# Optimization experiments

Hardware: AMD Instinct MI355X
Metric: run time of the kernel (lower is better)

The kernel has to match this reference:

```python
import jax, jax.numpy as jnp
import numpy as np

M, N, DIM, B = 64, 64, 512, 4096
SIGMA = max(M, N) / 2.0  # default sigma in BaseSOM.__init__


def setup_inputs() -> dict:
    key = jax.random.key(0)
    k1, k2 = jax.random.split(key)
    batch = jax.random.normal(k1, (B, DIM), dtype=jnp.float32)
    weights = jax.random.uniform(k2, (M * N, DIM), dtype=jnp.float32)
    # grid locations [(i, j) for i in range(M) for j in range(N)]
    ii, jj = jnp.meshgrid(jnp.arange(M), jnp.arange(N), indexing="ij")
    locations = jnp.stack([ii.reshape(-1), jj.reshape(-1)], axis=1).astype(jnp.int64)
    return {
        "batch": batch,
        "weights": weights,
        "locations": locations,
        "decay_rate": 1000,
        "it": 100,
    }


def reference(batch, weights, locations, decay_rate, it):
    # Squared Euclidean distances (argmin is identical to argmin of cdist p=2).
    x2 = jnp.sum(batch * batch, axis=1, keepdims=True)          # [B, 1]
    w2 = jnp.sum(weights * weights, axis=1)[None, :]            # [1, MN]
    d2 = x2 - 2.0 * (batch @ weights.T) + w2                    # [B, MN]
    bmu_indices = jnp.argmin(d2, axis=1)                        # [B]
    bmu_loc = locations[bmu_indices]                            # [B, 2]
    lr = jnp.exp(-jnp.float32(it) / jnp.float32(decay_rate))
    sigma_op = jnp.float32(SIGMA) * lr
    # [B, MN, 2] grid offsets -> squared grid distance [B, MN]
    diff = locations[None, :, :].astype(jnp.float32) - bmu_loc[:, None, :].astype(jnp.float32)
    dist_sq = jnp.sum(diff * diff, axis=2)
    return jnp.exp(-dist_sq / (sigma_op * sigma_op))
```

## Files before the change

### kernel.cpp

```cpp
#include <hip/hip_runtime.h>
#include <cfloat>

#define DIMK 512
#define MN   4096
#define BATCH 4096
#define BK 32
#define NGRP 1024

typedef _Float16 half8_t __attribute__((ext_vector_type(8)));
typedef _Float16 half4_t __attribute__((ext_vector_type(4)));
typedef float f32x4 __attribute__((ext_vector_type(4)));

#define GLD16(gp, lp) __builtin_amdgcn_global_load_lds( \
    (const __attribute__((address_space(1))) void*)(gp), \
    (__attribute__((address_space(3))) void*)(lp), 16, 0, 0)

__global__ __launch_bounds__(256) void convert_kernel(
        const float* __restrict__ X, const float* __restrict__ W,
        _Float16* __restrict__ Xh, _Float16* __restrict__ Wh,
        float* __restrict__ w2, float* __restrict__ xnorm) {
    const int blk  = blockIdx.x;
    const int t    = threadIdx.x;
    const bool isW = blk >= 1024;
    const float* src = isW ? W : X;
    _Float16* dst  = isW ? Wh : Xh;
    const int rblk = isW ? blk - 1024 : blk;
    const size_t idx = (size_t)rblk * 2048 + (size_t)t * 8;

    float4 v0 = *(const float4*)(src + idx);
    float4 v1 = *(const float4*)(src + idx + 4);
    float v[8] = {v0.x, v0.y, v0.z, v0.w, v1.x, v1.y, v1.z, v1.w};
    half8_t hv;
    float s = 0.f;
#pragma unroll
    for (int e = 0; e < 8; e++) {
        s += v[e] * v[e];
        hv[e] = (_Float16)v[e];
    }
    *(half8_t*)(dst + idx) = hv;
#pragma unroll
    for (int o = 32; o > 0; o >>= 1) s += __shfl_down(s, o);
    if ((t & 63) == 0) {
        int row = rblk * 4 + (t >> 6);
        if (isW) w2[row] = s;
        else     xnorm[row] = __fsqrt_rn(s);
    }
}

__global__ __launch_bounds__(256, 4) void score_kernel(
        const _Float16* __restrict__ Xh, const _Float16* __restrict__ Wh,
        const float* __restrict__ w2, float* __restrict__ Gm ) {
    __shared__ __align__(16) _Float16 lds[2][8192];

    const int t    = threadIdx.x;
    const int lane = t & 63;
    const int w    = t >> 6;
    const int wm   = w >> 1;
    const int wn   = w & 1;
    const int m0   = blockIdx.y * 128;
    const int n0   = blockIdx.x * 128;

    f32x4 acc[4][4];
#pragma unroll
    for (int i = 0; i < 4; i++)
#pragma unroll
        for (int j = 0; j < 4; j++) acc[i][j] = (f32x4){0.f, 0.f, 0.f, 0.f};

    const int r16 = lane & 15;
    const int kg  = lane >> 4;
    const int b0  = 2 * w, b1 = 2 * w + 1;
    const size_t ko = (size_t)kg * 8;
    const _Float16* gA0 = Xh + (size_t)(m0 + b0 * 16 + r16) * DIMK + ko;
    const _Float16* gA1 = Xh + (size_t)(m0 + b1 * 16 + r16) * DIMK + ko;
    const _Float16* gB0 = Wh + (size_t)(n0 + b0 * 16 + r16) * DIMK + ko;
    const _Float16* gB1 = Wh + (size_t)(n0 + b1 * 16 + r16) * DIMK + ko;
    const int dA0 = b0 * 512,        dA1 = b1 * 512;
    const int dB0 = 4096 + b0 * 512, dB1 = 4096 + b1 * 512;

    GLD16(gA0, &lds[0][dA0]);
    GLD16(gA1, &lds[0][dA1]);
    GLD16(gB0, &lds[0][dB0]);
    GLD16(gB1, &lds[0][dB1]);

    int cur = 0;
    for (int k0 = 0; k0 < DIMK; k0 += BK) {
        __syncthreads();
        if (k0 + BK < DIMK) {
            int nk = k0 + BK;
            GLD16(gA0 + nk, &lds[cur ^ 1][dA0]);
            GLD16(gA1 + nk, &lds[cur ^ 1][dA1]);
            GLD16(gB0 + nk, &lds[cur ^ 1][dB0]);
            GLD16(gB1 + nk, &lds[cur ^ 1][dB1]);
        }
        const _Float16* sA = &lds[cur][0];
        const _Float16* sB = &lds[cur][4096];

        half8_t ah[4], bh[4];
#pragma unroll
        for (int i = 0; i < 4; i++) {
            ah[i] = *(const half8_t*)(sA + (wm * 4 + i) * 512 + lane * 8);
            bh[i] = *(const half8_t*)(sB + (wn * 4 + i) * 512 + lane * 8);
        }
#pragma unroll
        for (int i = 0; i < 4; i++)
#pragma unroll
            for (int j = 0; j < 4; j++)
                acc[i][j] = __builtin_amdgcn_mfma_f32_16x16x32_f16(ah[i], bh[j], acc[i][j], 0, 0, 0);
        cur ^= 1;
    }

    const int q   = lane >> 4;
    const int cl  = lane & 15;
    const int gb  = (n0 >> 2) + wn * 16;
    float w2v[4];
#pragma unroll
    for (int j = 0; j < 4; j++) w2v[j] = w2[n0 + wn * 64 + j * 16 + cl];
#pragma unroll
    for (int i = 0; i < 4; i++)
#pragma unroll
        for (int v = 0; v < 4; v++) {
            const int row = m0 + wm * 64 + i * 16 + q * 4 + v;
            _Float16* grow = (_Float16*)Gm + (size_t)row * 8192 + gb;
#pragma unroll
            for (int j = 0; j < 4; j++) {
                float s = w2v[j] - 2.0f * acc[i][j][v];
                s = fminf(s, __shfl_xor(s, 1));
                s = fminf(s, __shfl_xor(s, 2));
                if ((cl & 3) == 0) grow[j * 4 + (cl >> 2)] = (_Float16)s;
            }
        }
}

__global__ __launch_bounds__(256) void epilogue_kernel(
        const float* __restrict__ w2, const float* __restrict__ xnorm,
        const float* __restrict__ X, const float* __restrict__ W,
        const int* __restrict__ decay_p, const int* __restrict__ it_p,
        float* out) {
    __shared__ float xs[512];
    __shared__ int   list[NGRP];
    __shared__ int   cnt;
    __shared__ float wmin[4];
    __shared__ float svv[4];
    __shared__ int   svi[4];
    __shared__ float tab[128];
    const int row  = blockIdx.x;
    const int t    = threadIdx.x;
    const int lane = t & 63;
    const int w    = t >> 6;

    {
        float2 xv = *(const float2*)(X + (size_t)row * DIMK + t * 2);
        xs[2 * t]     = xv.x;
        xs[2 * t + 1] = xv.y;
    }
    if (t == 0) cnt = 0;

    half4_t gmh = *((const half4_t*)((const _Float16*)out + (size_t)row * 8192) + t);
    float gme[4] = {(float)gmh[0], (float)gmh[1], (float)gmh[2], (float)gmh[3]};
    float g = fminf(fminf(gme[0], gme[1]), fminf(gme[2], gme[3]));
#pragma unroll
    for (int mask = 1; mask <= 32; mask <<= 1)
        g = fminf(g, __shfl_xor(g, mask));
    if (lane == 0) wmin[w] = g;
    __syncthreads();
    const float gmin = fminf(fminf(wmin[0], wmin[1]), fminf(wmin[2], wmin[3]));
    const float tau  = gmin + 2.0f * (0.0222f * xnorm[row] + 0.25f);

#pragma unroll
    for (int e = 0; e < 4; e++)
        if (gme[e] <= tau) list[atomicAdd(&cnt, 1)] = t * 4 + e;
    __syncthreads();
    const int total = cnt;

    float mbv = FLT_MAX;
    int   mbi = 0x7FFFFFFF;
    for (int idx = w; idx < total; idx += 4) {
        const int gid = list[idx];
#pragma unroll
        for (int cj = 0; cj < 4; cj++) {
            const int col = gid * 4 + cj;
            const float* wr = W + (size_t)col * DIMK;
            float p = 0.f;
#pragma unroll
            for (int e = 0; e < 8; e++) p += xs[lane * 8 + e] * wr[lane * 8 + e];
#pragma unroll
            for (int mask = 1; mask <= 32; mask <<= 1) p += __shfl_xor(p, mask);
            float s = w2[col] - 2.0f * p;
            if (s < mbv || (s == mbv && col < mbi)) { mbv = s; mbi = col; }
        }
    }
    if (lane == 0) { svv[w] = mbv; svi[w] = mbi; }
    __syncthreads();
    float sbv = svv[0]; int sbi = svi[0];
#pragma unroll
    for (int k = 1; k < 4; k++) {
        float s = svv[k]; int c = svi[k];
        if (s < sbv || (s == sbv && c < sbi)) { sbv = s; sbi = c; }
    }

    const float lr  = __expf(-(float)(*it_p) / (float)(*decay_p));
    const float so  = 32.0f * lr;
    const float inv = 1.0f / (so * so);
    const int rr = sbi >> 6, cc = sbi & 63;
    if (t < 64) {
        float d = (float)(t - rr);
        tab[t] = __expf(-d * d * inv);
    } else if (t < 128) {
        float d = (float)(t - 64 - cc);
        tab[t] = __expf(-d * d * inv);
    }
    __syncthreads();
    const float* er = tab;
    const float* ec = tab + 64;
    f32x4* orow = (f32x4*)(out + (size_t)row * 4096);
#pragma unroll
    for (int qq = 0; qq < 4; qq++) {
        int f  = qq * 256 + t;
        int i  = f >> 4;
        int j0 = (f & 15) * 4;
        float e = er[i];
        f32x4 o = {e * ec[j0], e * ec[j0 + 1], e * ec[j0 + 2], e * ec[j0 + 3]};
        __builtin_nontemporal_store(o, orow + f);
    }
}

extern "C" void kernel_launch(void* const* d_in, const int* in_sizes, int n_in,
                              void* d_out, int out_size, void* d_ws, size_t ws_size,
                              hipStream_t stream) {
    const float* X       = (const float*)d_in[0];
    const float* W       = (const float*)d_in[1];
    const int*   decay_p = (const int*)d_in[3];
    const int*   it_p    = (const int*)d_in[4];
    float* out = (float*)d_out;

    _Float16* Xh = (_Float16*)d_ws;
    _Float16* Wh = Xh + (size_t)BATCH * DIMK;
    float*    w2 = (float*)(Wh + (size_t)MN * DIMK);
    float*    xn = w2 + MN;

    convert_kernel<<<2048, 256, 0, stream>>>(X, W, Xh, Wh, w2, xn);
    score_kernel<<<dim3(32, 32), 256, 0, stream>>>(Xh, Wh, w2, out);
    epilogue_kernel<<<BATCH, 256, 0, stream>>>(w2, xn, X, W, decay_p, it_p, out);
}
```

Measured before the change: 146.2 us.

## Enlarge score GEMM tile to 256x256 with phased MFMA schedule and XCD-aware block mapping

```diff
diff --git a/kernel.cpp b/kernel.cpp
--- a/kernel.cpp
+++ b/kernel.cpp
@@ -4,7 +4,6 @@
 #define DIMK 512
 #define MN   4096
 #define BATCH 4096
-#define BK 32
 #define NGRP 1024
 
 typedef _Float16 half8_t __attribute__((ext_vector_type(8)));
@@ -47,66 +46,114 @@
     }
 }
 
-__global__ __launch_bounds__(256, 4) void score_kernel(
+#define MFMA_HALF(R) \
+    do { \
+        acc[(R)+0][0] = __builtin_amdgcn_mfma_f32_16x16x32_f16(ah0, bh0, acc[(R)+0][0], 0, 0, 0); \
+        acc[(R)+0][1] = __builtin_amdgcn_mfma_f32_16x16x32_f16(ah0, bh1, acc[(R)+0][1], 0, 0, 0); \
+        acc[(R)+0][2] = __builtin_amdgcn_mfma_f32_16x16x32_f16(ah0, bh2, acc[(R)+0][2], 0, 0, 0); \
+        acc[(R)+0][3] = __builtin_amdgcn_mfma_f32_16x16x32_f16(ah0, bh3, acc[(R)+0][3], 0, 0, 0); \
+        acc[(R)+1][0] = __builtin_amdgcn_mfma_f32_16x16x32_f16(ah1, bh0, acc[(R)+1][0], 0, 0, 0); \
+        acc[(R)+1][1] = __builtin_amdgcn_mfma_f32_16x16x32_f16(ah1, bh1, acc[(R)+1][1], 0, 0, 0); \
+        acc[(R)+1][2] = __builtin_amdgcn_mfma_f32_16x16x32_f16(ah1, bh2, acc[(R)+1][2], 0, 0, 0); \
+        acc[(R)+1][3] = __builtin_amdgcn_mfma_f32_16x16x32_f16(ah1, bh3, acc[(R)+1][3], 0, 0, 0); \
+        acc[(R)+2][0] = __builtin_amdgcn_mfma_f32_16x16x32_f16(ah2, bh0, acc[(R)+2][0], 0, 0, 0); \
+        acc[(R)+2][1] = __builtin_amdgcn_mfma_f32_16x16x32_f16(ah2, bh1, acc[(R)+2][1], 0, 0, 0); \
+        acc[(R)+2][2] = __builtin_amdgcn_mfma_f32_16x16x32_f16(ah2, bh2, acc[(R)+2][2], 0, 0, 0); \
+        acc[(R)+2][3] = __builtin_amdgcn_mfma_f32_16x16x32_f16(ah2, bh3, acc[(R)+2][3], 0, 0, 0); \
+        acc[(R)+3][0] = __builtin_amdgcn_mfma_f32_16x16x32_f16(ah3, bh0, acc[(R)+3][0], 0, 0, 0); \
+        acc[(R)+3][1] = __builtin_amdgcn_mfma_f32_16x16x32_f16(ah3, bh1, acc[(R)+3][1], 0, 0, 0); \
+        acc[(R)+3][2] = __builtin_amdgcn_mfma_f32_16x16x32_f16(ah3, bh2, acc[(R)+3][2], 0, 0, 0); \
+        acc[(R)+3][3] = __builtin_amdgcn_mfma_f32_16x16x32_f16(ah3, bh3, acc[(R)+3][3], 0, 0, 0); \
+    } while (0)
+
+#define PHASE_TAIL(R) \
+    do { \
+        __builtin_amdgcn_s_barrier(); \
+        asm volatile("s_waitcnt lgkmcnt(0)" ::: "memory"); \
+        __builtin_amdgcn_sched_barrier(0); \
+        __builtin_amdgcn_s_setprio(1); \
+        MFMA_HALF(R); \
+        __builtin_amdgcn_s_setprio(0); \
+        __builtin_amdgcn_s_barrier(); \
+    } while (0)
+
+__global__ __launch_bounds__(512, 2) void score_kernel(
         const _Float16* __restrict__ Xh, const _Float16* __restrict__ Wh,
         const float* __restrict__ w2, float* __restrict__ Gm ) {
-    __shared__ __align__(16) _Float16 lds[2][8192];
+    __shared__ __align__(16) _Float16 lds[2][2][16384];
 
     const int t    = threadIdx.x;
     const int lane = t & 63;
     const int w    = t >> 6;
-    const int wm   = w >> 1;
-    const int wn   = w & 1;
-    const int m0   = blockIdx.y * 128;
-    const int n0   = blockIdx.x * 128;
-
-    f32x4 acc[4][4];
-#pragma unroll
-    for (int i = 0; i < 4; i++)
+    const int wm   = w >> 2;
+    const int wn   = w & 3;
+
+    const int id  = blockIdx.y * 16 + blockIdx.x;
+    const int xcd = id & 7;
+    const int li  = id >> 3;
+    const int bm  = (xcd >> 1) * 4 + (li >> 3);
+    const int bn  = (xcd & 1) * 8 + (li & 7);
+    const int m0  = bm * 256;
+    const int n0  = bn * 256;
+
+    const int srow = ((t >> 7) << 4) + (t & 15);
+    const int skof = ((t >> 6) & 1) * 32 + ((t >> 4) & 3) * 8;
+    const _Float16* gA = Xh + (size_t)(m0 + srow) * DIMK + skof;
+    const _Float16* gB = Wh + (size_t)(n0 + srow) * DIMK + skof;
+    const int ldst = t * 8;
+
+#define STG_A(b, kt, c) GLD16(gA + (size_t)(c) * (64 * DIMK) + (kt) * 64, &lds[b][0][(c) * 4096 + ldst])
+#define STG_B(b, kt, c) GLD16(gB + (size_t)(c) * (64 * DIMK) + (kt) * 64, &lds[b][1][(c) * 4096 + ldst])
+#define LDA(b, rg, ks) (*(const half8_t*)(&lds[b][0][(rg) * 1024 + (ks) * 512 + lane * 8]))
+#define LDB(b, rg, ks) (*(const half8_t*)(&lds[b][1][(rg) * 1024 + (ks) * 512 + lane * 8]))
+
+    f32x4 acc[8][4];
+#pragma unroll
+    for (int i = 0; i < 8; i++)
 #pragma unroll
         for (int j = 0; j < 4; j++) acc[i][j] = (f32x4){0.f, 0.f, 0.f, 0.f};
 
-    const int r16 = lane & 15;
-    const int kg  = lane >> 4;
-    const int b0  = 2 * w, b1 = 2 * w + 1;
-    const size_t ko = (size_t)kg * 8;
-    const _Float16* gA0 = Xh + (size_t)(m0 + b0 * 16 + r16) * DIMK + ko;
-    const _Float16* gA1 = Xh + (size_t)(m0 + b1 * 16 + r16) * DIMK + ko;
-    const _Float16* gB0 = Wh + (size_t)(n0 + b0 * 16 + r16) * DIMK + ko;
-    const _Float16* gB1 = Wh + (size_t)(n0 + b1 * 16 + r16) * DIMK + ko;
-    const int dA0 = b0 * 512,        dA1 = b1 * 512;
-    const int dB0 = 4096 + b0 * 512, dB1 = 4096 + b1 * 512;
-
-    GLD16(gA0, &lds[0][dA0]);
-    GLD16(gA1, &lds[0][dA1]);
-    GLD16(gB0, &lds[0][dB0]);
-    GLD16(gB1, &lds[0][dB1]);
-
-    int cur = 0;
-    for (int k0 = 0; k0 < DIMK; k0 += BK) {
-        __syncthreads();
-        if (k0 + BK < DIMK) {
-            int nk = k0 + BK;
-            GLD16(gA0 + nk, &lds[cur ^ 1][dA0]);
-            GLD16(gA1 + nk, &lds[cur ^ 1][dA1]);
-            GLD16(gB0 + nk, &lds[cur ^ 1][dB0]);
-            GLD16(gB1 + nk, &lds[cur ^ 1][dB1]);
+    STG_A(0, 0, 0); STG_A(0, 0, 1); STG_A(0, 0, 2); STG_A(0, 0, 3);
+    STG_B(0, 0, 0); STG_B(0, 0, 1); STG_B(0, 0, 2); STG_B(0, 0, 3);
+
+    half8_t ah0, ah1, ah2, ah3, bh0, bh1, bh2, bh3;
+
+    for (int kt = 0; kt < 8; ++kt) {
+        const int  b  = kt & 1;
+        const int  nb = b ^ 1;
+        const bool dn = kt < 7;
+
+        if (dn) {
+            STG_A(nb, kt + 1, 0); STG_A(nb, kt + 1, 1);
+            asm volatile("s_waitcnt vmcnt(2)" ::: "memory");
+        } else {
+            asm volatile("s_waitcnt vmcnt(0)" ::: "memory");
         }
-        const _Float16* sA = &lds[cur][0];
-        const _Float16* sB = &lds[cur][4096];
-
-        half8_t ah[4], bh[4];
-#pragma unroll
-        for (int i = 0; i < 4; i++) {
-            ah[i] = *(const half8_t*)(sA + (wm * 4 + i) * 512 + lane * 8);
-            bh[i] = *(const half8_t*)(sB + (wn * 4 + i) * 512 + lane * 8);
-        }
-#pragma unroll
-        for (int i = 0; i < 4; i++)
-#pragma unroll
-            for (int j = 0; j < 4; j++)
-                acc[i][j] = __builtin_amdgcn_mfma_f32_16x16x32_f16(ah[i], bh[j], acc[i][j], 0, 0, 0);
-        cur ^= 1;
+        __builtin_amdgcn_sched_barrier(0);
+        __builtin_amdgcn_s_barrier();
+
+        ah0 = LDA(b, wm * 8 + 0, 0); ah1 = LDA(b, wm * 8 + 1, 0);
+        ah2 = LDA(b, wm * 8 + 2, 0); ah3 = LDA(b, wm * 8 + 3, 0);
+        bh0 = LDB(b, wn * 4 + 0, 0); bh1 = LDB(b, wn * 4 + 1, 0);
+        bh2 = LDB(b, wn * 4 + 2, 0); bh3 = LDB(b, wn * 4 + 3, 0);
+        if (dn) { STG_A(nb, kt + 1, 2); STG_A(nb, kt + 1, 3); }
+        PHASE_TAIL(0);
+
+        ah0 = LDA(b, wm * 8 + 4, 0); ah1 = LDA(b, wm * 8 + 5, 0);
+        ah2 = LDA(b, wm * 8 + 6, 0); ah3 = LDA(b, wm * 8 + 7, 0);
+        if (dn) { STG_B(nb, kt + 1, 0); STG_B(nb, kt + 1, 1); }
+        PHASE_TAIL(4);
+
+        ah0 = LDA(b, wm * 8 + 0, 1); ah1 = LDA(b, wm * 8 + 1, 1);
+        ah2 = LDA(b, wm * 8 + 2, 1); ah3 = LDA(b, wm * 8 + 3, 1);
+        bh0 = LDB(b, wn * 4 + 0, 1); bh1 = LDB(b, wn * 4 + 1, 1);
+        bh2 = LDB(b, wn * 4 + 2, 1); bh3 = LDB(b, wn * 4 + 3, 1);
+        if (dn) { STG_B(nb, kt + 1, 2); STG_B(nb, kt + 1, 3); }
+        PHASE_TAIL(0);
+
+        ah0 = LDA(b, wm * 8 + 4, 1); ah1 = LDA(b, wm * 8 + 5, 1);
+        ah2 = LDA(b, wm * 8 + 6, 1); ah3 = LDA(b, wm * 8 + 7, 1);
+        PHASE_TAIL(4);
     }
 
     const int q   = lane >> 4;
@@ -116,14 +163,14 @@
 #pragma unroll
     for (int j = 0; j < 4; j++) w2v[j] = w2[n0 + wn * 64 + j * 16 + cl];
 #pragma unroll
-    for (int i = 0; i < 4; i++)
+    for (int ai = 0; ai < 8; ai++)
 #pragma unroll
         for (int v = 0; v < 4; v++) {
-            const int row = m0 + wm * 64 + i * 16 + q * 4 + v;
+            const int row = m0 + wm * 128 + ai * 16 + q * 4 + v;
             _Float16* grow = (_Float16*)Gm + (size_t)row * 8192 + gb;
 #pragma unroll
             for (int j = 0; j < 4; j++) {
-                float s = w2v[j] - 2.0f * acc[i][j][v];
+                float s = w2v[j] - 2.0f * acc[ai][j][v];
                 s = fminf(s, __shfl_xor(s, 1));
                 s = fminf(s, __shfl_xor(s, 2));
                 if ((cl & 3) == 0) grow[j * 4 + (cl >> 2)] = (_Float16)s;
@@ -239,6 +286,6 @@
     float*    xn = w2 + MN;
 
     convert_kernel<<<2048, 256, 0, stream>>>(X, W, Xh, Wh, w2, xn);
-    score_kernel<<<dim3(32, 32), 256, 0, stream>>>(Xh, Wh, w2, out);
+    score_kernel<<<dim3(16, 16), 512, 0, stream>>>(Xh, Wh, w2, out);
     epilogue_kernel<<<BATCH, 256, 0, stream>>>(w2, xn, X, W, decay_p, it_p, out);
 }
```

New measurement: 134.6 us. -7.9%, faster.
